# Optimization experiments

Hardware: AMD Instinct MI355X
Metric: run time of the kernel (lower is better)

The kernel has to match this reference:

```python
import jax, jax.numpy as jnp
import numpy as np

B, A, C = 128, 8732, 21
ALPHA = 1.0
NEG_POS_RATIO = 3


def setup_inputs() -> dict:
    key = jax.random.key(0)
    k1, k2, k3, k4, k5 = jax.random.split(key, 5)
    confidences = jax.random.normal(k1, (B, A, C), dtype=jnp.float32)
    locations = jax.random.normal(k2, (B, A, 4), dtype=jnp.float32)
    gt_locations = jax.random.normal(k3, (B, A, 4), dtype=jnp.float32)
    raw_cls = jax.random.randint(k4, (B, A), 1, C)
    is_pos = jax.random.uniform(k5, (B, A)) < 0.03
    gt_labels = jnp.where(is_pos, raw_cls, 0).astype(jnp.int32)
    return {
        "confidences": confidences,
        "locations": locations,
        "gt_labels": gt_labels,
        "gt_locations": gt_locations,
    }


def reference(confidences, locations, gt_labels, gt_locations):
    pos_mask = gt_labels > 0                     # (B, A)
    neg_avail = gt_labels == 0                   # (B, A)

    # smooth L1 (beta=1) summed over positive anchors
    d = locations - gt_locations                 # (B, A, 4)
    ad = jnp.abs(d)
    sl1 = jnp.where(ad < 1.0, 0.5 * d * d, ad - 0.5)
    loc_loss = jnp.sum(sl1 * pos_mask[..., None].astype(sl1.dtype))

    # per-anchor cross entropy
    logp = jax.nn.log_softmax(confidences, axis=-1)              # (B, A, C)
    ce = -jnp.take_along_axis(logp, gt_labels[..., None].astype(jnp.int32), axis=-1)[..., 0]  # (B, A)

    # hard negative mining: top-(3*num_pos) CE among negatives, per row
    num_pos = jnp.sum(pos_mask, axis=1)                          # (B,)
    num_neg = jnp.minimum(NEG_POS_RATIO * num_pos, jnp.sum(neg_avail, axis=1))
    ce_neg = jnp.where(pos_mask, 0.0, ce)                        # zero out positives (CE >= 0)
    order = jnp.argsort(-ce_neg, axis=1)                         # descending
    ranks = jnp.argsort(order, axis=1)                           # rank of each anchor in descending order
    neg_mask = ranks < num_neg[:, None]

    keep = pos_mask | neg_mask
    conf_loss = jnp.sum(jnp.where(keep, ce, 0.0))

    total_loss = (loc_loss + ALPHA * conf_loss) / jnp.sum(num_pos).astype(loc_loss.dtype)
    return total_loss
```

## Files before the change

kernel.cpp:

```cpp
#include <hip/hip_runtime.h>
#include <math.h>

#define B_ 128
#define A_ 8732
#define C_ 21
#define APB 256
#define NBLK ((A_ + APB - 1) / APB)
#define NPART (B_ * NBLK)
#define KPT 35

#define OFF_PLOC 0
#define OFF_PPCE 17920
#define OFF_PNP  35840
#define OFF_RCN  53760
#define OFF_RNP  54272
#define OFF_CEN  57344

__global__ __launch_bounds__(256) void k_ce(
        const float* __restrict__ conf, const float* __restrict__ loc,
        const int* __restrict__ lab, const float* __restrict__ gloc,
        float* __restrict__ ce_neg, float* __restrict__ part_loc,
        float* __restrict__ part_pce, int* __restrict__ part_np)
{
    __shared__ float sConf[APB * C_];
    const int b   = blockIdx.y;
    const int a0  = blockIdx.x * APB;
    const int n   = min(APB, A_ - a0);
    const int tid = threadIdx.x;

    {
        const size_t base = ((size_t)b * A_ + a0) * C_;
        const int n4 = (n * C_) >> 2;
        const float4* src4 = (const float4*)(conf + base);
        float4* dst4 = (float4*)sConf;
        #pragma unroll
        for (int j = 0; j < 6; j++) {
            const int i = tid + j * 256;
            if (i < n4) dst4[i] = src4[i];
        }
    }
    __syncthreads();

    float pce = 0.f, lloss = 0.f;
    int pcnt = 0;
    if (tid < n) {
        const int a = a0 + tid;
        float v[C_];
        #pragma unroll
        for (int j = 0; j < C_; j++) v[j] = sConf[tid * C_ + j];
        float m = v[0];
        #pragma unroll
        for (int j = 1; j < C_; j++) m = fmaxf(m, v[j]);
        float s = 0.f;
        #pragma unroll
        for (int j = 0; j < C_; j++) s += __expf(v[j] - m);
        const int L = lab[(size_t)b * A_ + a];
        const float ce = __logf(s) + m - v[L];
        const bool pos = (L > 0);
        ce_neg[(size_t)b * A_ + a] = pos ? 0.f : ce;
        if (pos) {
            pce = ce;
            pcnt = 1;
            const float4 lv = ((const float4*)loc)[(size_t)b * A_ + a];
            const float4 gv = ((const float4*)gloc)[(size_t)b * A_ + a];
            float dx = lv.x - gv.x, dy = lv.y - gv.y, dz = lv.z - gv.z, dw = lv.w - gv.w;
            float ax = fabsf(dx), ay = fabsf(dy), az = fabsf(dz), aw = fabsf(dw);
            lloss  = (ax < 1.f) ? 0.5f * dx * dx : ax - 0.5f;
            lloss += (ay < 1.f) ? 0.5f * dy * dy : ay - 0.5f;
            lloss += (az < 1.f) ? 0.5f * dz * dz : az - 0.5f;
            lloss += (aw < 1.f) ? 0.5f * dw * dw : aw - 0.5f;
        }
    }

    #pragma unroll
    for (int off = 32; off > 0; off >>= 1) {
        pce   += __shfl_down(pce, off);
        lloss += __shfl_down(lloss, off);
        pcnt  += __shfl_down(pcnt, off);
    }
    __shared__ float wf[4], wl[4];
    __shared__ int wc[4];
    const int wave = tid >> 6, lane = tid & 63;
    if (lane == 0) { wf[wave] = pce; wl[wave] = lloss; wc[wave] = pcnt; }
    __syncthreads();
    if (tid == 0) {
        const int bid = b * NBLK + blockIdx.x;
        part_loc[bid] = wl[0] + wl[1] + wl[2] + wl[3];
        part_pce[bid] = wf[0] + wf[1] + wf[2] + wf[3];
        part_np[bid]  = wc[0] + wc[1] + wc[2] + wc[3];
    }
}

__global__ __launch_bounds__(256) void k_select(
        const float* __restrict__ ce_neg, const int* __restrict__ part_np,
        float* __restrict__ row_cneg, int* __restrict__ row_np)
{
    const int b = blockIdx.x;
    const int tid = threadIdx.x;
    const int wave = tid >> 6, lane = tid & 63;
    const float* ce = ce_neg + (size_t)b * A_;

    __shared__ unsigned long long shCnt[4];
    __shared__ float shS[4];
    __shared__ int shNp, shK, shMode;
    __shared__ unsigned shLo, shHi;

    unsigned keys[KPT];
    #pragma unroll
    for (int j = 0; j < KPT; j++) {
        const int i = tid + j * 256;
        keys[j] = (i < A_) ? __float_as_uint(ce[i]) : 0u;
    }

    if (wave == 0) {
        int v = (lane < NBLK) ? part_np[b * NBLK + lane] : 0;
        #pragma unroll
        for (int off = 32; off > 0; off >>= 1) v += __shfl_down(v, off);
        if (lane == 0) shNp = v;
    }

    {
        unsigned c0 = 0; float s0 = 0.f;
        #pragma unroll
        for (int j = 0; j < KPT; j++)
            if (keys[j]) { c0++; s0 += __uint_as_float(keys[j]); }
        #pragma unroll
        for (int off = 32; off > 0; off >>= 1) {
            c0 += __shfl_down(c0, off);
            s0 += __shfl_down(s0, off);
        }
        if (lane == 0) { shCnt[wave] = c0; shS[wave] = s0; }
    }
    __syncthreads();
    if (tid == 0) {
        const int np = shNp;
        const int k = min(3 * np, A_ - np);
        const unsigned cnt0 = (unsigned)(shCnt[0] + shCnt[1] + shCnt[2] + shCnt[3]);
        const float sum0 = shS[0] + shS[1] + shS[2] + shS[3];
        row_np[b] = np;
        if (k <= 0)                    { shMode = 2; row_cneg[b] = 0.f; }
        else if (cnt0 < (unsigned)k)   { shMode = 2; row_cneg[b] = sum0; }
        else { shMode = 0; shK = k; shLo = 0u; shHi = 0x42800000u; }
    }
    __syncthreads();
    if (shMode == 2) return;

    const int k = shK;
    unsigned lo = shLo, hi = shHi;
    while (hi - lo > 1u) {
        const unsigned w = hi - lo;
        unsigned m1, m2, m3;
        if (w >= 4u) { const unsigned q = w >> 2; m1 = lo + q; m2 = lo + 2*q; m3 = lo + 3*q; }
        else         { m1 = m2 = m3 = lo + (w >> 1); }
        unsigned c1 = 0, c2 = 0, c3 = 0;
        #pragma unroll
        for (int j = 0; j < KPT; j++) {
            c1 += (unsigned)__popcll(__ballot(keys[j] > m1));
            c2 += (unsigned)__popcll(__ballot(keys[j] > m2));
            c3 += (unsigned)__popcll(__ballot(keys[j] > m3));
        }
        if (lane == 0)
            shCnt[wave] = (unsigned long long)c1
                        | ((unsigned long long)c2 << 16)
                        | ((unsigned long long)c3 << 32);
        __syncthreads();
        if (tid == 0) {
            const unsigned long long t = shCnt[0] + shCnt[1] + shCnt[2] + shCnt[3];
            const int C1 = (int)(t & 0xFFFF), C2 = (int)((t >> 16) & 0xFFFF),
                      C3 = (int)((t >> 32) & 0xFFFF);
            unsigned nlo, nhi;
            if      (C3 >= k) { nlo = m3; nhi = hi; }
            else if (C2 >= k) { nlo = m2; nhi = m3; }
            else if (C1 >= k) { nlo = m1; nhi = m2; }
            else              { nlo = lo; nhi = m1; }
            shLo = nlo; shHi = nhi;
        }
        __syncthreads();
        lo = shLo; hi = shHi;
    }

    const unsigned kth = hi;
    unsigned c = 0; float s = 0.f;
    #pragma unroll
    for (int j = 0; j < KPT; j++)
        if (keys[j] > kth) { c++; s += __uint_as_float(keys[j]); }
    #pragma unroll
    for (int off = 32; off > 0; off >>= 1) {
        c += __shfl_down(c, off);
        s += __shfl_down(s, off);
    }
    if (lane == 0) { shCnt[wave] = c; shS[wave] = s; }
    __syncthreads();
    if (tid == 0) {
        const unsigned Cg = (unsigned)(shCnt[0] + shCnt[1] + shCnt[2] + shCnt[3]);
        const float Sg = shS[0] + shS[1] + shS[2] + shS[3];
        row_cneg[b] = Sg + (float)(k - (int)Cg) * __uint_as_float(kth);
    }
}

__global__ __launch_bounds__(1024) void k_final(
        const float* __restrict__ part_loc, const float* __restrict__ part_pce,
        const float* __restrict__ row_cneg, const int* __restrict__ row_np,
        float* __restrict__ out)
{
    const int tid = threadIdx.x;
    const int wave = tid >> 6, lane = tid & 63;
    float s = 0.f;
    for (int i = tid; i < NPART; i += 1024) s += part_loc[i] + part_pce[i];
    int n = 0;
    if (tid < B_) { s += row_cneg[tid]; n = row_np[tid]; }
    #pragma unroll
    for (int off = 32; off > 0; off >>= 1) {
        s += __shfl_down(s, off);
        n += __shfl_down(n, off);
    }
    __shared__ float ws_[16];
    __shared__ int wn_[16];
    if (lane == 0) { ws_[wave] = s; wn_[wave] = n; }
    __syncthreads();
    if (tid == 0) {
        float S = 0.f; int N = 0;
        #pragma unroll
        for (int w = 0; w < 16; w++) { S += ws_[w]; N += wn_[w]; }
        out[0] = S / (float)N;
    }
}

extern "C" void kernel_launch(void* const* d_in, const int* in_sizes, int n_in,
                              void* d_out, int out_size, void* d_ws, size_t ws_size,
                              hipStream_t stream) {
    const float* conf = (const float*)d_in[0];
    const float* loc  = (const float*)d_in[1];
    const int*   lab  = (const int*)d_in[2];
    const float* gloc = (const float*)d_in[3];

    char* ws = (char*)d_ws;
    float* part_loc = (float*)(ws + OFF_PLOC);
    float* part_pce = (float*)(ws + OFF_PPCE);
    int*   part_np  = (int*)(ws + OFF_PNP);
    float* row_cneg = (float*)(ws + OFF_RCN);
    int*   row_np   = (int*)(ws + OFF_RNP);
    float* ce_neg   = (float*)(ws + OFF_CEN);

    dim3 g1(NBLK, B_);
    k_ce<<<g1, 256, 0, stream>>>(conf, loc, lab, gloc, ce_neg,
                                 part_loc, part_pce, part_np);
    k_select<<<B_, 256, 0, stream>>>(ce_neg, part_np, row_cneg, row_np);
    k_final<<<1, 1024, 0, stream>>>(part_loc, part_pce, row_cneg, row_np,
                                    (float*)d_out);
}
```

Measured before the change: 212.3 us.

## Widen k_select to 1024 threads with redundant per-thread reduction and double-buffered counts

The hard-negative selection kernel now runs 1024 threads per row instead of 256, so each thread holds 9 keys instead of 35. The per-iteration tid==0 decision step and its second barrier are removed: every thread reads all 16 wave counts from a double-buffered shared array and updates its own search bounds, leaving one barrier per bisection step. Counting moves to wave ballots instead of per-thread counters plus shuffles. The aim is to cut the latency of the serial search, at the cost of each thread summing 16 shared entries every step.

```diff
diff --git a/kernel.cpp b/kernel.cpp
--- a/kernel.cpp
+++ b/kernel.cpp
@@ -7,7 +7,7 @@
 #define APB 256
 #define NBLK ((A_ + APB - 1) / APB)
 #define NPART (B_ * NBLK)
-#define KPT 35
+#define KPT 9
 
 #define OFF_PLOC 0
 #define OFF_PPCE 17920
@@ -91,7 +91,7 @@
     }
 }
 
-__global__ __launch_bounds__(256) void k_select(
+__global__ __launch_bounds__(1024, 2) void k_select(
         const float* __restrict__ ce_neg, const int* __restrict__ part_np,
         float* __restrict__ row_cneg, int* __restrict__ row_np)
 {
@@ -100,15 +100,14 @@
     const int wave = tid >> 6, lane = tid & 63;
     const float* ce = ce_neg + (size_t)b * A_;
 
-    __shared__ unsigned long long shCnt[4];
-    __shared__ float shS[4];
-    __shared__ int shNp, shK, shMode;
-    __shared__ unsigned shLo, shHi;
+    __shared__ unsigned long long shCnt[2][16];
+    __shared__ float shS[16];
+    __shared__ int shNp;
 
     unsigned keys[KPT];
     #pragma unroll
     for (int j = 0; j < KPT; j++) {
-        const int i = tid + j * 256;
+        const int i = tid + j * 1024;
         keys[j] = (i < A_) ? __float_as_uint(ce[i]) : 0u;
     }
 
@@ -122,31 +121,30 @@
     {
         unsigned c0 = 0; float s0 = 0.f;
         #pragma unroll
-        for (int j = 0; j < KPT; j++)
-            if (keys[j]) { c0++; s0 += __uint_as_float(keys[j]); }
-        #pragma unroll
-        for (int off = 32; off > 0; off >>= 1) {
-            c0 += __shfl_down(c0, off);
-            s0 += __shfl_down(s0, off);
-        }
-        if (lane == 0) { shCnt[wave] = c0; shS[wave] = s0; }
-    }
-    __syncthreads();
-    if (tid == 0) {
-        const int np = shNp;
-        const int k = min(3 * np, A_ - np);
-        const unsigned cnt0 = (unsigned)(shCnt[0] + shCnt[1] + shCnt[2] + shCnt[3]);
-        const float sum0 = shS[0] + shS[1] + shS[2] + shS[3];
-        row_np[b] = np;
-        if (k <= 0)                    { shMode = 2; row_cneg[b] = 0.f; }
-        else if (cnt0 < (unsigned)k)   { shMode = 2; row_cneg[b] = sum0; }
-        else { shMode = 0; shK = k; shLo = 0u; shHi = 0x42800000u; }
-    }
-    __syncthreads();
-    if (shMode == 2) return;
-
-    const int k = shK;
-    unsigned lo = shLo, hi = shHi;
+        for (int j = 0; j < KPT; j++) {
+            c0 += (unsigned)__popcll(__ballot(keys[j] != 0u));
+            s0 += __uint_as_float(keys[j]);
+        }
+        #pragma unroll
+        for (int off = 32; off > 0; off >>= 1) s0 += __shfl_down(s0, off);
+        if (lane == 0) { shCnt[0][wave] = c0; shS[wave] = s0; }
+    }
+    __syncthreads();
+
+    const int np = shNp;
+    const int k = min(3 * np, A_ - np);
+    unsigned cnt0 = 0; float sum0 = 0.f;
+    #pragma unroll
+    for (int w = 0; w < 16; w++) { cnt0 += (unsigned)shCnt[0][w]; sum0 += shS[w]; }
+
+    if (k <= 0) { if (tid == 0) { row_cneg[b] = 0.f; row_np[b] = np; } return; }
+    if (cnt0 < (unsigned)k) {
+        if (tid == 0) { row_cneg[b] = sum0; row_np[b] = np; }
+        return;
+    }
+
+    unsigned lo = 0u, hi = 0x42800000u;
+    int p = 1;
     while (hi - lo > 1u) {
         const unsigned w = hi - lo;
         unsigned m1, m2, m3;
@@ -160,41 +158,39 @@
             c3 += (unsigned)__popcll(__ballot(keys[j] > m3));
         }
         if (lane == 0)
-            shCnt[wave] = (unsigned long long)c1
-                        | ((unsigned long long)c2 << 16)
-                        | ((unsigned long long)c3 << 32);
+            shCnt[p][wave] = (unsigned long long)c1
+                           | ((unsigned long long)c2 << 16)
+                           | ((unsigned long long)c3 << 32);
         __syncthreads();
-        if (tid == 0) {
-            const unsigned long long t = shCnt[0] + shCnt[1] + shCnt[2] + shCnt[3];
-            const int C1 = (int)(t & 0xFFFF), C2 = (int)((t >> 16) & 0xFFFF),
-                      C3 = (int)((t >> 32) & 0xFFFF);
-            unsigned nlo, nhi;
-            if      (C3 >= k) { nlo = m3; nhi = hi; }
-            else if (C2 >= k) { nlo = m2; nhi = m3; }
-            else if (C1 >= k) { nlo = m1; nhi = m2; }
-            else              { nlo = lo; nhi = m1; }
-            shLo = nlo; shHi = nhi;
-        }
-        __syncthreads();
-        lo = shLo; hi = shHi;
+        unsigned long long t = 0;
+        #pragma unroll
+        for (int w2 = 0; w2 < 16; w2++) t += shCnt[p][w2];
+        const int C1 = (int)(t & 0xFFFF), C2 = (int)((t >> 16) & 0xFFFF),
+                  C3 = (int)((t >> 32) & 0xFFFF);
+        if      (C3 >= k) { lo = m3; }
+        else if (C2 >= k) { lo = m2; hi = m3; }
+        else if (C1 >= k) { lo = m1; hi = m2; }
+        else              { hi = m1; }
+        p ^= 1;
     }
 
     const unsigned kth = hi;
     unsigned c = 0; float s = 0.f;
     #pragma unroll
-    for (int j = 0; j < KPT; j++)
-        if (keys[j] > kth) { c++; s += __uint_as_float(keys[j]); }
-    #pragma unroll
-    for (int off = 32; off > 0; off >>= 1) {
-        c += __shfl_down(c, off);
-        s += __shfl_down(s, off);
-    }
-    if (lane == 0) { shCnt[wave] = c; shS[wave] = s; }
+    for (int j = 0; j < KPT; j++) {
+        c += (unsigned)__popcll(__ballot(keys[j] > kth));
+        s += (keys[j] > kth) ? __uint_as_float(keys[j]) : 0.f;
+    }
+    #pragma unroll
+    for (int off = 32; off > 0; off >>= 1) s += __shfl_down(s, off);
+    if (lane == 0) { shCnt[0][wave] = c; shS[wave] = s; }
     __syncthreads();
     if (tid == 0) {
-        const unsigned Cg = (unsigned)(shCnt[0] + shCnt[1] + shCnt[2] + shCnt[3]);
-        const float Sg = shS[0] + shS[1] + shS[2] + shS[3];
+        unsigned Cg = 0; float Sg = 0.f;
+        #pragma unroll
+        for (int w = 0; w < 16; w++) { Cg += (unsigned)shCnt[0][w]; Sg += shS[w]; }
         row_cneg[b] = Sg + (float)(k - (int)Cg) * __uint_as_float(kth);
+        row_np[b] = np;
     }
 }
 
@@ -245,7 +241,7 @@
     dim3 g1(NBLK, B_);
     k_ce<<<g1, 256, 0, stream>>>(conf, loc, lab, gloc, ce_neg,
                                  part_loc, part_pce, part_np);
-    k_select<<<B_, 256, 0, stream>>>(ce_neg, part_np, row_cneg, row_np);
+    k_select<<<B_, 1024, 0, stream>>>(ce_neg, part_np, row_cneg, row_np);
     k_final<<<1, 1024, 0, stream>>>(part_loc, part_pce, row_cneg, row_np,
                                     (float*)d_out);
 }
```

After: 188.9 us. -11.0%, faster.
